# Optimization experiments

Measured on AMD Instinct MI355X. Metric: run time of the kernel, lower is better.

Reference implementation:

```python
import jax, jax.numpy as jnp
import numpy as np
import math

PHI = (1.0 + math.sqrt(5.0)) / 2.0
LUT_SIZE = 4096
TWO_PI = 2.0 * math.pi


def _lut_tables():
    # 4096-entry sin/cos lookup tables over [0, 2*pi)
    grid = jnp.arange(LUT_SIZE, dtype=jnp.float32) * (TWO_PI / LUT_SIZE)
    return jnp.sin(grid), jnp.cos(grid)


def _lookup_sin_cos(theta, sin_t, cos_t):
    # nearest-entry LUT lookup: index = round(theta / (2*pi) * N) mod N
    idx = jnp.mod(jnp.round(theta * (LUT_SIZE / TWO_PI)), LUT_SIZE).astype(jnp.int32)
    return sin_t[idx], cos_t[idx]


def setup_inputs() -> dict:
    key = jax.random.key(0)
    ks = jax.random.split(key, 6)
    B, D, H = 16, 2048, 2048
    return {
        "current_state_real": jax.random.normal(ks[0], (B, D), jnp.float32),
        "current_state_imag": jax.random.normal(ks[1], (B, D), jnp.float32),
        "history_real": jax.random.normal(ks[2], (B, H, D), jnp.float32),
        "history_imag": jax.random.normal(ks[3], (B, H, D), jnp.float32),
        "ema_state": jax.random.normal(ks[4], (B, 2 * D), jnp.float32),
        "w_q": jax.random.normal(ks[5], (D,), jnp.float32) * 0.02,
        "b_q": jnp.zeros((D,), jnp.float32),
        "alpha": jnp.asarray(0.1, jnp.float32),
        "t": jnp.asarray(3.0, jnp.float32),
    }


def reference(current_state_real, current_state_imag, history_real, history_imag,
              ema_state, w_q, b_q, alpha, t):
    D = current_state_real.shape[-1]
    scale = math.sqrt(2.0 * D)
    sin_t, cos_t = _lut_tables()

    wl_q = 1.0 + jnp.abs(w_q)                      # (D,)
    t_phi = t * PHI
    theta_real = current_state_real / wl_q + b_q + t_phi   # (B, D)
    theta_imag = current_state_imag / wl_q + b_q + t_phi   # (B, D)
    _, cos_q_real = _lookup_sin_cos(theta_real, sin_t, cos_t)
    _, cos_q_imag = _lookup_sin_cos(theta_imag, sin_t, cos_t)

    # keys == values == stacked history (no projection): (B, H, 2D)
    keys = jnp.concatenate([history_real, history_imag], axis=-1)
    query_for_match = jnp.concatenate([cos_q_real, cos_q_imag], axis=-1)  # (B, 2D)

    scores = jnp.einsum('bd,bhd->bh', query_for_match, keys) / scale      # (B, H)
    weights = jax.nn.softmax(scores, axis=-1)
    retrieved = jnp.einsum('bh,bhd->bd', weights, keys)                   # (B, 2D)

    a = jax.nn.sigmoid(alpha)
    new_ema = a * retrieved + (1.0 - a) * ema_state
    return new_ema
```

## Files before the change

### kernel.cpp

```cpp
#include <hip/hip_runtime.h>
#include <math.h>

#ifndef M_PI
#define M_PI 3.14159265358979323846
#endif

#define LUT_N 4096
#define WPB 4

__device__ __forceinline__ float lut_cos(float theta) {
    const float IDX_SCALE = (float)((double)LUT_N / (2.0 * M_PI));
    const float STEP = (float)((2.0 * M_PI) / (double)LUT_N);
    float x = theta * IDX_SCALE;
    int i = (int)rintf(x);
    i &= (LUT_N - 1);
    return cosf((float)i * STEP);
}

__global__ void qgen_kernel(const float* __restrict__ cur_r,
                            const float* __restrict__ cur_i,
                            const float* __restrict__ w_q,
                            const float* __restrict__ b_q,
                            const float* __restrict__ t_ptr,
                            float* __restrict__ q_out,
                            int B, int D) {
    int idx = blockIdx.x * blockDim.x + threadIdx.x;
    int twoD = 2 * D;
    if (idx >= B * twoD) return;
    int b = idx / twoD;
    int c = idx - b * twoD;
    int col = (c < D) ? c : c - D;
    const float* src = (c < D) ? cur_r : cur_i;
    float v = src[(size_t)b * D + col];
    float t_phi = t_ptr[0] * 1.61803398874989484820f;
    float wl = 1.0f + fabsf(w_q[col]);
    float theta = v / wl + b_q[col] + t_phi;
    q_out[idx] = lut_cos(theta);
}

__global__ __launch_bounds__(256, 2) void flash_kernel(
    const float* __restrict__ hist_r,
    const float* __restrict__ hist_i,
    const float* __restrict__ q_ws,
    float* __restrict__ r_ws,
    float* __restrict__ ml_ws,
    int H, int S) {
    const int t = threadIdx.x;
    const int lane = t & 63;
    const int wv = t >> 6;
    const int b = blockIdx.x / S;
    const int s = blockIdx.x - b * S;
    const int rows_blk = H / S;
    const int R = rows_blk / WPB;
    const int h0 = s * rows_blk + wv * R;

    __shared__ float4 qsh[1024];
    __shared__ float4 sred[1024];
    __shared__ float sm[WPB], sl[WPB];

    const float4* q4 = (const float4*)q_ws + (size_t)b * 1024;
#pragma unroll
    for (int k = 0; k < 4; ++k) qsh[t + 256 * k] = q4[t + 256 * k];
    __syncthreads();

    const float4* hr = (const float4*)hist_r + ((size_t)b * H + h0) * 512 + lane;
    const float4* hi = (const float4*)hist_i + ((size_t)b * H + h0) * 512 + lane;

    float4 rv[16];
#pragma unroll
    for (int j = 0; j < 16; ++j) rv[j] = make_float4(0.f, 0.f, 0.f, 0.f);
    float m0 = -INFINITY, l = 0.f;
    const float inv_scale = 1.0f / 64.0f;

    for (int r = 0; r < R; ++r) {
        asm volatile("" ::: "memory");

        float4 kv[16];
#pragma unroll
        for (int j = 0; j < 8; ++j) kv[j] = hr[(size_t)r * 512 + j * 64];
#pragma unroll
        for (int j = 0; j < 8; ++j) kv[8 + j] = hi[(size_t)r * 512 + j * 64];

        float p = 0.f;
#pragma unroll
        for (int j = 0; j < 16; ++j) {
            float4 qv = qsh[j * 64 + lane];
            p += qv.x * kv[j].x + qv.y * kv[j].y +
                 qv.z * kv[j].z + qv.w * kv[j].w;
        }
#pragma unroll
        for (int off = 32; off; off >>= 1) p += __shfl_xor(p, off);
        float sc = p * inv_scale;

        float d = sc - m0;
        float w;
        if (d > 8.0f) {
            float corr = __expf(-d);
            l *= corr;
#pragma unroll
            for (int j = 0; j < 16; ++j) {
                rv[j].x *= corr; rv[j].y *= corr;
                rv[j].z *= corr; rv[j].w *= corr;
            }
            m0 = sc;
            w = 1.0f;
        } else {
            w = __expf(d);
        }
        l += w;
#pragma unroll
        for (int j = 0; j < 16; ++j) {
            rv[j].x = fmaf(w, kv[j].x, rv[j].x);
            rv[j].y = fmaf(w, kv[j].y, rv[j].y);
            rv[j].z = fmaf(w, kv[j].z, rv[j].z);
            rv[j].w = fmaf(w, kv[j].w, rv[j].w);
        }
    }

    if (lane == 0) { sm[wv] = m0; sl[wv] = l; }
    __syncthreads();
    float M = fmaxf(fmaxf(sm[0], sm[1]), fmaxf(sm[2], sm[3]));
    float Lb = sl[0] * __expf(sm[0] - M) + sl[1] * __expf(sm[1] - M) +
               sl[2] * __expf(sm[2] - M) + sl[3] * __expf(sm[3] - M);
    float scale = __expf(m0 - M);

    for (int w = 0; w < WPB; ++w) {
        if (wv == w) {
#pragma unroll
            for (int j = 0; j < 16; ++j) {
                int idx = j * 64 + lane;
                float4 v = (w == 0) ? make_float4(0.f, 0.f, 0.f, 0.f) : sred[idx];
                v.x = fmaf(scale, rv[j].x, v.x);
                v.y = fmaf(scale, rv[j].y, v.y);
                v.z = fmaf(scale, rv[j].z, v.z);
                v.w = fmaf(scale, rv[j].w, v.w);
                sred[idx] = v;
            }
        }
        __syncthreads();
    }

    float4* ro = (float4*)r_ws + (size_t)blockIdx.x * 1024;
#pragma unroll
    for (int k = 0; k < 4; ++k) ro[t + 256 * k] = sred[t + 256 * k];
    if (t == 0) {
        ml_ws[2 * (size_t)blockIdx.x] = M;
        ml_ws[2 * (size_t)blockIdx.x + 1] = Lb;
    }
}

__global__ void combine_kernel(const float* __restrict__ r_ws,
                               const float* __restrict__ ml_ws,
                               const float* __restrict__ ema,
                               const float* __restrict__ alpha_ptr,
                               float* __restrict__ out,
                               int D, int S) {
    const int twoD = 2 * D;
    const int nc = twoD / 256;
    const int b = blockIdx.x / nc;
    const int cb = blockIdx.x - b * nc;
    const int c = cb * 256 + threadIdx.x;

    const float* ml = ml_ws + (size_t)b * S * 2;
    float M = -INFINITY;
    for (int s = 0; s < S; ++s) M = fmaxf(M, ml[2 * s]);
    float L = 0.f;
    for (int s = 0; s < S; ++s) L += ml[2 * s + 1] * __expf(ml[2 * s] - M);

    float acc = 0.f;
    const float* rb = r_ws + (size_t)b * S * twoD + c;
    for (int s = 0; s < S; ++s)
        acc = fmaf(__expf(ml[2 * s] - M), rb[(size_t)s * twoD], acc);

    float a = 1.0f / (1.0f + __expf(-alpha_ptr[0]));
    float retrieved = acc / L;
    size_t o = (size_t)b * twoD + c;
    out[o] = a * retrieved + (1.0f - a) * ema[o];
}

extern "C" void kernel_launch(void* const* d_in, const int* in_sizes, int n_in,
                              void* d_out, int out_size, void* d_ws, size_t ws_size,
                              hipStream_t stream) {
    const float* cur_r  = (const float*)d_in[0];
    const float* cur_i  = (const float*)d_in[1];
    const float* hist_r = (const float*)d_in[2];
    const float* hist_i = (const float*)d_in[3];
    const float* ema    = (const float*)d_in[4];
    const float* w_q    = (const float*)d_in[5];
    const float* b_q    = (const float*)d_in[6];
    const float* alpha  = (const float*)d_in[7];
    const float* t      = (const float*)d_in[8];

    const int D = in_sizes[5];
    const int B = in_sizes[0] / D;
    const int H = in_sizes[2] / (B * D);
    const int twoD = 2 * D;

    float* q_ws = (float*)d_ws;
    size_t q_elems = (size_t)B * twoD;

    int S = 32;
    while (S > 1) {
        size_t need = (q_elems + (size_t)B * S * twoD + (size_t)B * S * 2) * sizeof(float);
        if (need <= ws_size) break;
        S >>= 1;
    }
    float* r_ws = q_ws + q_elems;
    float* ml_ws = r_ws + (size_t)B * S * twoD;

    int qblocks = (B * twoD + 255) / 256;
    qgen_kernel<<<qblocks, 256, 0, stream>>>(cur_r, cur_i, w_q, b_q, t, q_ws, B, D);
    flash_kernel<<<B * S, 256, 0, stream>>>(hist_r, hist_i, q_ws, r_ws, ml_ws, H, S);
    combine_kernel<<<B * (twoD / 256), 256, 0, stream>>>(r_ws, ml_ws, ema, alpha,
                                                         (float*)d_out, D, S);
}
```

Before: 123.7 us.

## Double-buffer history rows with inline-asm loads and shared-memory accumulators

Restructures the flash kernel to use 2 waves per block and many more blocks (768/B per batch). Each wave takes history rows strided across all waves. Row loads are issued through inline global_load_dwordx4 with explicit vmcnt waits, so the next row is fetched while the current one is processed. The per-wave output accumulator moves from registers into LDS, which frees VGPRs for the two in-flight row buffers. The aim is to hide HBM latency on this bandwidth-bound 536MB stream, at the cost of extra LDS read-modify-write traffic per row and a larger combine step.

```diff
diff --git a/kernel.cpp b/kernel.cpp
--- a/kernel.cpp
+++ b/kernel.cpp
@@ -6,7 +6,7 @@
 #endif
 
 #define LUT_N 4096
-#define WPB 4
+#define WVS 2
 
 __device__ __forceinline__ float lut_cos(float theta) {
     const float IDX_SCALE = (float)((double)LUT_N / (2.0 * M_PI));
@@ -38,111 +38,152 @@
     q_out[idx] = lut_cos(theta);
 }
 
-__global__ __launch_bounds__(256, 2) void flash_kernel(
+__device__ __forceinline__ void issue_row(float4 (&kv)[16],
+                                          const float* hr_row,
+                                          const float* hi_row, int lane) {
+#pragma unroll
+    for (int j = 0; j < 8; ++j)
+        asm volatile("global_load_dwordx4 %0, %1, off"
+                     : "=&v"(kv[j])
+                     : "v"(hr_row + j * 256 + lane * 4));
+#pragma unroll
+    for (int j = 0; j < 8; ++j)
+        asm volatile("global_load_dwordx4 %0, %1, off"
+                     : "=&v"(kv[8 + j])
+                     : "v"(hi_row + j * 256 + lane * 4));
+}
+
+#define WAITV(N) do { \
+    asm volatile("s_waitcnt vmcnt(" #N ")" ::: "memory"); \
+    __builtin_amdgcn_sched_barrier(0); } while (0)
+
+__device__ __forceinline__ void proc_row(const float4 (&kv)[16],
+                                         const float4* qsh,
+                                         float4* rp,
+                                         int lane, float& m0, float& l) {
+    float p0 = 0.f, p1 = 0.f, p2 = 0.f, p3 = 0.f;
+#pragma unroll
+    for (int k = 0; k < 4; ++k) {
+        float4 qa = qsh[(4 * k + 0) * 64 + lane];
+        float4 qb = qsh[(4 * k + 1) * 64 + lane];
+        float4 qc = qsh[(4 * k + 2) * 64 + lane];
+        float4 qd = qsh[(4 * k + 3) * 64 + lane];
+        p0 += qa.x * kv[4*k+0].x + qa.y * kv[4*k+0].y +
+              qa.z * kv[4*k+0].z + qa.w * kv[4*k+0].w;
+        p1 += qb.x * kv[4*k+1].x + qb.y * kv[4*k+1].y +
+              qb.z * kv[4*k+1].z + qb.w * kv[4*k+1].w;
+        p2 += qc.x * kv[4*k+2].x + qc.y * kv[4*k+2].y +
+              qc.z * kv[4*k+2].z + qc.w * kv[4*k+2].w;
+        p3 += qd.x * kv[4*k+3].x + qd.y * kv[4*k+3].y +
+              qd.z * kv[4*k+3].z + qd.w * kv[4*k+3].w;
+    }
+    float p = (p0 + p1) + (p2 + p3);
+#pragma unroll
+    for (int off = 32; off; off >>= 1) p += __shfl_xor(p, off);
+    float sc = p * (1.0f / 64.0f);
+
+    float d = sc - m0;
+    float w;
+    if (d > 8.0f) {
+        float corr = __expf(-d);
+        l *= corr;
+#pragma unroll
+        for (int k = 0; k < 16; ++k) {
+            float4 v = rp[k * 64 + lane];
+            v.x *= corr; v.y *= corr; v.z *= corr; v.w *= corr;
+            rp[k * 64 + lane] = v;
+        }
+        m0 = sc;
+        w = 1.0f;
+    } else {
+        w = __expf(d);
+    }
+    l += w;
+#pragma unroll
+    for (int k = 0; k < 16; ++k) {
+        float4 v = rp[k * 64 + lane];
+        v.x = fmaf(w, kv[k].x, v.x);
+        v.y = fmaf(w, kv[k].y, v.y);
+        v.z = fmaf(w, kv[k].z, v.z);
+        v.w = fmaf(w, kv[k].w, v.w);
+        rp[k * 64 + lane] = v;
+    }
+}
+
+__global__ __launch_bounds__(128, 2) void flash_kernel(
     const float* __restrict__ hist_r,
     const float* __restrict__ hist_i,
     const float* __restrict__ q_ws,
     float* __restrict__ r_ws,
     float* __restrict__ ml_ws,
-    int H, int S) {
+    int H, int Wb, int bpb) {
     const int t = threadIdx.x;
     const int lane = t & 63;
     const int wv = t >> 6;
-    const int b = blockIdx.x / S;
-    const int s = blockIdx.x - b * S;
-    const int rows_blk = H / S;
-    const int R = rows_blk / WPB;
-    const int h0 = s * rows_blk + wv * R;
+    const int b = blockIdx.x / bpb;
+    const int j = (blockIdx.x - b * bpb) * WVS + wv;
 
     __shared__ float4 qsh[1024];
-    __shared__ float4 sred[1024];
-    __shared__ float sm[WPB], sl[WPB];
+    __shared__ float4 rvb[WVS][1024];
+    __shared__ float sm[WVS], sl[WVS];
 
     const float4* q4 = (const float4*)q_ws + (size_t)b * 1024;
 #pragma unroll
-    for (int k = 0; k < 4; ++k) qsh[t + 256 * k] = q4[t + 256 * k];
+    for (int k = 0; k < 8; ++k) qsh[t + 128 * k] = q4[t + 128 * k];
+    float4* rp = &rvb[wv][0];
+#pragma unroll
+    for (int k = 0; k < 16; ++k)
+        rp[k * 64 + lane] = make_float4(0.f, 0.f, 0.f, 0.f);
     __syncthreads();
 
-    const float4* hr = (const float4*)hist_r + ((size_t)b * H + h0) * 512 + lane;
-    const float4* hi = (const float4*)hist_i + ((size_t)b * H + h0) * 512 + lane;
-
-    float4 rv[16];
-#pragma unroll
-    for (int j = 0; j < 16; ++j) rv[j] = make_float4(0.f, 0.f, 0.f, 0.f);
+    const int n = (H - j + Wb - 1) / Wb;
+    const size_t step = (size_t)Wb * 2048;
+    const float* hr = hist_r + ((size_t)b * H + j) * 2048;
+    const float* hi = hist_i + ((size_t)b * H + j) * 2048;
+
     float m0 = -INFINITY, l = 0.f;
-    const float inv_scale = 1.0f / 64.0f;
-
-    for (int r = 0; r < R; ++r) {
-        asm volatile("" ::: "memory");
-
-        float4 kv[16];
-#pragma unroll
-        for (int j = 0; j < 8; ++j) kv[j] = hr[(size_t)r * 512 + j * 64];
-#pragma unroll
-        for (int j = 0; j < 8; ++j) kv[8 + j] = hi[(size_t)r * 512 + j * 64];
-
-        float p = 0.f;
-#pragma unroll
-        for (int j = 0; j < 16; ++j) {
-            float4 qv = qsh[j * 64 + lane];
-            p += qv.x * kv[j].x + qv.y * kv[j].y +
-                 qv.z * kv[j].z + qv.w * kv[j].w;
-        }
-#pragma unroll
-        for (int off = 32; off; off >>= 1) p += __shfl_xor(p, off);
-        float sc = p * inv_scale;
-
-        float d = sc - m0;
-        float w;
-        if (d > 8.0f) {
-            float corr = __expf(-d);
-            l *= corr;
-#pragma unroll
-            for (int j = 0; j < 16; ++j) {
-                rv[j].x *= corr; rv[j].y *= corr;
-                rv[j].z *= corr; rv[j].w *= corr;
-            }
-            m0 = sc;
-            w = 1.0f;
-        } else {
-            w = __expf(d);
-        }
-        l += w;
-#pragma unroll
-        for (int j = 0; j < 16; ++j) {
-            rv[j].x = fmaf(w, kv[j].x, rv[j].x);
-            rv[j].y = fmaf(w, kv[j].y, rv[j].y);
-            rv[j].z = fmaf(w, kv[j].z, rv[j].z);
-            rv[j].w = fmaf(w, kv[j].w, rv[j].w);
-        }
+    float4 kvA[16], kvB[16];
+    if (n > 0) issue_row(kvA, hr, hi, lane);
+    if (n > 1) issue_row(kvB, hr + step, hi + step, lane);
+
+    int i = 0;
+    for (; i + 2 < n; i += 2) {
+        WAITV(16);
+        proc_row(kvA, qsh, rp, lane, m0, l);
+        issue_row(kvA, hr + (size_t)(i + 2) * step, hi + (size_t)(i + 2) * step, lane);
+        WAITV(16);
+        proc_row(kvB, qsh, rp, lane, m0, l);
+        if (i + 3 < n)
+            issue_row(kvB, hr + (size_t)(i + 3) * step, hi + (size_t)(i + 3) * step, lane);
+    }
+    if (n - i == 2) {
+        WAITV(16);
+        proc_row(kvA, qsh, rp, lane, m0, l);
+        WAITV(0);
+        proc_row(kvB, qsh, rp, lane, m0, l);
+    } else if (n - i == 1) {
+        WAITV(0);
+        proc_row(kvA, qsh, rp, lane, m0, l);
     }
 
     if (lane == 0) { sm[wv] = m0; sl[wv] = l; }
     __syncthreads();
-    float M = fmaxf(fmaxf(sm[0], sm[1]), fmaxf(sm[2], sm[3]));
-    float Lb = sl[0] * __expf(sm[0] - M) + sl[1] * __expf(sm[1] - M) +
-               sl[2] * __expf(sm[2] - M) + sl[3] * __expf(sm[3] - M);
+    float M = fmaxf(sm[0], sm[1]);
+    float Lb = sl[0] * __expf(sm[0] - M) + sl[1] * __expf(sm[1] - M);
     float scale = __expf(m0 - M);
-
-    for (int w = 0; w < WPB; ++w) {
-        if (wv == w) {
-#pragma unroll
-            for (int j = 0; j < 16; ++j) {
-                int idx = j * 64 + lane;
-                float4 v = (w == 0) ? make_float4(0.f, 0.f, 0.f, 0.f) : sred[idx];
-                v.x = fmaf(scale, rv[j].x, v.x);
-                v.y = fmaf(scale, rv[j].y, v.y);
-                v.z = fmaf(scale, rv[j].z, v.z);
-                v.w = fmaf(scale, rv[j].w, v.w);
-                sred[idx] = v;
-            }
-        }
-        __syncthreads();
-    }
+#pragma unroll
+    for (int k = 0; k < 16; ++k) {
+        float4 v = rp[k * 64 + lane];
+        v.x *= scale; v.y *= scale; v.z *= scale; v.w *= scale;
+        rp[k * 64 + lane] = v;
+    }
+    __syncthreads();
 
     float4* ro = (float4*)r_ws + (size_t)blockIdx.x * 1024;
-#pragma unroll
-    for (int k = 0; k < 4; ++k) ro[t + 256 * k] = sred[t + 256 * k];
+    for (int k = t; k < 1024; k += 128) {
+        float4 a = rvb[0][k], c = rvb[1][k];
+        ro[k] = make_float4(a.x + c.x, a.y + c.y, a.z + c.z, a.w + c.w);
+    }
     if (t == 0) {
         ml_ws[2 * (size_t)blockIdx.x] = M;
         ml_ws[2 * (size_t)blockIdx.x + 1] = Lb;
@@ -199,18 +240,20 @@
     float* q_ws = (float*)d_ws;
     size_t q_elems = (size_t)B * twoD;
 
-    int S = 32;
-    while (S > 1) {
-        size_t need = (q_elems + (size_t)B * S * twoD + (size_t)B * S * 2) * sizeof(float);
+    int bpb = 768 / B; if (bpb < 1) bpb = 1;
+    while (bpb > 1) {
+        size_t need = (q_elems + (size_t)B * bpb * twoD + (size_t)B * bpb * 2) * sizeof(float);
         if (need <= ws_size) break;
-        S >>= 1;
-    }
+        bpb >>= 1;
+    }
+    const int Wb = bpb * WVS;
     float* r_ws = q_ws + q_elems;
-    float* ml_ws = r_ws + (size_t)B * S * twoD;
+    float* ml_ws = r_ws + (size_t)B * bpb * twoD;
 
     int qblocks = (B * twoD + 255) / 256;
     qgen_kernel<<<qblocks, 256, 0, stream>>>(cur_r, cur_i, w_q, b_q, t, q_ws, B, D);
-    flash_kernel<<<B * S, 256, 0, stream>>>(hist_r, hist_i, q_ws, r_ws, ml_ws, H, S);
+    flash_kernel<<<B * bpb, WVS * 64, 0, stream>>>(hist_r, hist_i, q_ws, r_ws, ml_ws,
+                                                   H, Wb, bpb);
     combine_kernel<<<B * (twoD / 256), 256, 0, stream>>>(r_ws, ml_ws, ema, alpha,
-                                                         (float*)d_out, D, S);
-}
+                                                         (float*)d_out, D, bpb);
+}
```

After: 143.2 us. +15.8%, slower.

## Fuse query generation into flash kernel, share LDS, store partials as bf16

Applied to the files above, without the earlier changes.

Drops the separate qgen kernel: each flash block now computes the LUT-cosine query for its batch row straight into shared memory. The query buffer and the reduction buffer share one LDS array, which halves shared memory and lets launch bounds request 4 blocks per CU instead of 2. Per-split partial results are written to the workspace as bf16 and widened in the combine kernel, cutting partial-result traffic. In exchange every block recomputes the query, including cosf calls, and the partials lose precision.

```diff
diff --git a/kernel.cpp b/kernel.cpp
--- a/kernel.cpp
+++ b/kernel.cpp
@@ -1,4 +1,5 @@
 #include <hip/hip_runtime.h>
+#include <hip/hip_bf16.h>
 #include <math.h>
 
 #ifndef M_PI
@@ -17,32 +18,15 @@
     return cosf((float)i * STEP);
 }
 
-__global__ void qgen_kernel(const float* __restrict__ cur_r,
-                            const float* __restrict__ cur_i,
-                            const float* __restrict__ w_q,
-                            const float* __restrict__ b_q,
-                            const float* __restrict__ t_ptr,
-                            float* __restrict__ q_out,
-                            int B, int D) {
-    int idx = blockIdx.x * blockDim.x + threadIdx.x;
-    int twoD = 2 * D;
-    if (idx >= B * twoD) return;
-    int b = idx / twoD;
-    int c = idx - b * twoD;
-    int col = (c < D) ? c : c - D;
-    const float* src = (c < D) ? cur_r : cur_i;
-    float v = src[(size_t)b * D + col];
-    float t_phi = t_ptr[0] * 1.61803398874989484820f;
-    float wl = 1.0f + fabsf(w_q[col]);
-    float theta = v / wl + b_q[col] + t_phi;
-    q_out[idx] = lut_cos(theta);
-}
-
-__global__ __launch_bounds__(256, 2) void flash_kernel(
+__global__ __launch_bounds__(256, 4) void flash_kernel(
+    const float* __restrict__ cur_r,
+    const float* __restrict__ cur_i,
+    const float* __restrict__ w_q,
+    const float* __restrict__ b_q,
+    const float* __restrict__ t_ptr,
     const float* __restrict__ hist_r,
     const float* __restrict__ hist_i,
-    const float* __restrict__ q_ws,
-    float* __restrict__ r_ws,
+    __hip_bfloat16* __restrict__ r_ws,
     float* __restrict__ ml_ws,
     int H, int S) {
     const int t = threadIdx.x;
@@ -54,14 +38,24 @@
     const int R = rows_blk / WPB;
     const int h0 = s * rows_blk + wv * R;
 
-    __shared__ float4 qsh[1024];
-    __shared__ float4 sred[1024];
+    __shared__ float qshf[4096];
     __shared__ float sm[WPB], sl[WPB];
 
-    const float4* q4 = (const float4*)q_ws + (size_t)b * 1024;
-#pragma unroll
-    for (int k = 0; k < 4; ++k) qsh[t + 256 * k] = q4[t + 256 * k];
+    {
+        const float t_phi = t_ptr[0] * 1.61803398874989484820f;
+#pragma unroll
+        for (int k = 0; k < 16; ++k) {
+            int c = t + 256 * k;
+            int col = c & 2047;
+            float v = (c < 2048) ? cur_r[(size_t)b * 2048 + col]
+                                 : cur_i[(size_t)b * 2048 + col];
+            float wl = 1.0f + fabsf(w_q[col]);
+            float theta = v / wl + b_q[col] + t_phi;
+            qshf[c] = lut_cos(theta);
+        }
+    }
     __syncthreads();
+    const float4* qsh = (const float4*)qshf;
 
     const float4* hr = (const float4*)hist_r + ((size_t)b * H + h0) * 512 + lane;
     const float4* hi = (const float4*)hist_i + ((size_t)b * H + h0) * 512 + lane;
@@ -117,6 +111,7 @@
         }
     }
 
+    __syncthreads();
     if (lane == 0) { sm[wv] = m0; sl[wv] = l; }
     __syncthreads();
     float M = fmaxf(fmaxf(sm[0], sm[1]), fmaxf(sm[2], sm[3]));
@@ -124,6 +119,7 @@
                sl[2] * __expf(sm[2] - M) + sl[3] * __expf(sm[3] - M);
     float scale = __expf(m0 - M);
 
+    float4* sred = (float4*)qshf;
     for (int w = 0; w < WPB; ++w) {
         if (wv == w) {
 #pragma unroll
@@ -140,16 +136,24 @@
         __syncthreads();
     }
 
-    float4* ro = (float4*)r_ws + (size_t)blockIdx.x * 1024;
-#pragma unroll
-    for (int k = 0; k < 4; ++k) ro[t + 256 * k] = sred[t + 256 * k];
+    ushort4* ro = (ushort4*)(r_ws + (size_t)blockIdx.x * 4096);
+#pragma unroll
+    for (int k = 0; k < 4; ++k) {
+        float4 v = sred[t + 256 * k];
+        union { ushort4 u; __hip_bfloat16 h[4]; } cvt;
+        cvt.h[0] = __float2bfloat16(v.x);
+        cvt.h[1] = __float2bfloat16(v.y);
+        cvt.h[2] = __float2bfloat16(v.z);
+        cvt.h[3] = __float2bfloat16(v.w);
+        ro[t + 256 * k] = cvt.u;
+    }
     if (t == 0) {
         ml_ws[2 * (size_t)blockIdx.x] = M;
         ml_ws[2 * (size_t)blockIdx.x + 1] = Lb;
     }
 }
 
-__global__ void combine_kernel(const float* __restrict__ r_ws,
+__global__ void combine_kernel(const __hip_bfloat16* __restrict__ r_ws,
                                const float* __restrict__ ml_ws,
                                const float* __restrict__ ema,
                                const float* __restrict__ alpha_ptr,
@@ -168,9 +172,10 @@
     for (int s = 0; s < S; ++s) L += ml[2 * s + 1] * __expf(ml[2 * s] - M);
 
     float acc = 0.f;
-    const float* rb = r_ws + (size_t)b * S * twoD + c;
+    const __hip_bfloat16* rb = r_ws + (size_t)b * S * twoD + c;
     for (int s = 0; s < S; ++s)
-        acc = fmaf(__expf(ml[2 * s] - M), rb[(size_t)s * twoD], acc);
+        acc = fmaf(__expf(ml[2 * s] - M),
+                   __bfloat162float(rb[(size_t)s * twoD]), acc);
 
     float a = 1.0f / (1.0f + __expf(-alpha_ptr[0]));
     float retrieved = acc / L;
@@ -196,21 +201,20 @@
     const int H = in_sizes[2] / (B * D);
     const int twoD = 2 * D;
 
-    float* q_ws = (float*)d_ws;
-    size_t q_elems = (size_t)B * twoD;
-
     int S = 32;
     while (S > 1) {
-        size_t need = (q_elems + (size_t)B * S * twoD + (size_t)B * S * 2) * sizeof(float);
+        size_t need = (size_t)B * S * twoD * sizeof(__hip_bfloat16) + 256
+                    + (size_t)B * S * 2 * sizeof(float);
         if (need <= ws_size) break;
         S >>= 1;
     }
-    float* r_ws = q_ws + q_elems;
-    float* ml_ws = r_ws + (size_t)B * S * twoD;
-
-    int qblocks = (B * twoD + 255) / 256;
-    qgen_kernel<<<qblocks, 256, 0, stream>>>(cur_r, cur_i, w_q, b_q, t, q_ws, B, D);
-    flash_kernel<<<B * S, 256, 0, stream>>>(hist_r, hist_i, q_ws, r_ws, ml_ws, H, S);
+    __hip_bfloat16* r_ws = (__hip_bfloat16*)d_ws;
+    size_t r_bytes = (size_t)B * S * twoD * sizeof(__hip_bfloat16);
+    r_bytes = (r_bytes + 255) & ~(size_t)255;
+    float* ml_ws = (float*)((char*)d_ws + r_bytes);
+
+    flash_kernel<<<B * S, 256, 0, stream>>>(cur_r, cur_i, w_q, b_q, t,
+                                            hist_r, hist_i, r_ws, ml_ws, H, S);
     combine_kernel<<<B * (twoD / 256), 256, 0, stream>>>(r_ws, ml_ws, ema, alpha,
                                                          (float*)d_out, D, S);
 }
```

After: 186.7 us. +51.0%, slower.
